# Kernel tuning notes

Hardware: AMD Instinct MI355X
Metric: run time of the kernel (lower is better)

The kernel has to match this reference:

```python
import jax, jax.numpy as jnp
import numpy as np

N, J, P = 512, 20000, 8   # samples, genes (rna_count), covariates
DIM = J - 1               # pivot=True drops one column from the softmax logits


def setup_inputs() -> dict:
    key = jax.random.key(0)
    k0, k1, k2, k3, k4 = jax.random.split(key, 5)
    X = jax.random.normal(k0, (N, P), dtype=jnp.float32)
    # counts: non-negative integers stored as float (matches torch float64 Y of counts)
    Y = jnp.round(jax.random.uniform(k1, (N, J), dtype=jnp.float32) * 1000.0)
    mu = jax.random.normal(k2, (DIM,), dtype=jnp.float32)
    beta = jax.random.normal(k3, (P * DIM,), dtype=jnp.float32) * 0.1
    phi = jax.random.normal(k4, (J,), dtype=jnp.float32)
    return {"mu": mu, "beta": beta, "phi": phi, "X": X, "Y": Y}


def _nb_loglik(y, mean, disp):
    # NB with mean `mean` and dispersion `disp` (var = mean + disp*mean^2):
    # r = 1/disp, p = r/(r+mean)
    # log pmf = lgamma(y+r) - lgamma(r) - lgamma(y+1) + r*log(p) + y*log(1-p)
    r = 1.0 / disp
    log_rpm = jnp.log(r + mean)
    return (jax.lax.lgamma(y + r) - jax.lax.lgamma(r) - jax.lax.lgamma(y + 1.0)
            + r * (jnp.log(r) - log_rpm)
            + y * (jnp.log(mean) - log_rpm))


def reference(mu, beta, phi, X, Y):
    n, p = X.shape
    dim = mu.shape[0]
    beta_ = beta.reshape(p, dim)
    logits = mu + X @ beta_                                   # [N, J-1]
    logits = jnp.concatenate(
        [logits, jnp.zeros((n, 1), dtype=logits.dtype)], axis=1)  # pivot column of zeros -> [N, J]
    pi = jax.nn.softmax(logits, axis=1)                       # exp(logits - logsumexp)
    s = jnp.sum(Y, axis=1, keepdims=True)                     # [N, 1] total counts per sample
    mean = s * pi                                             # [N, J]
    disp = jax.nn.softplus(phi)                               # [J]
    log_lik = jnp.sum(_nb_loglik(Y, mean, disp))
    return log_lik.reshape(1)
```

## Files before the change

### kernel.cpp

```cpp
#include <hip/hip_runtime.h>
#include <hip/hip_bf16.h>

constexpr int N_SAMPLES = 512;
constexpr int J_GENES   = 20000;
constexpr int P_COV     = 8;
constexpr int DIM       = J_GENES - 1;
constexpr int BLOCK     = 256;
constexpr int CHUNK     = 1024;
constexpr int CPR       = (J_GENES + CHUNK - 1) / CHUNK;
constexpr int TABLE_N   = 1024;

constexpr size_t WS_RW    = 0;
constexpr size_t WS_LOGRW = WS_RW    + J_GENES;
constexpr size_t WS_LGRW  = WS_LOGRW + J_GENES;
constexpr size_t WS_MUP   = WS_LGRW  + J_GENES;
constexpr size_t WS_BETAP = WS_MUP   + J_GENES;
constexpr size_t WS_LGYT  = WS_BETAP + (size_t)P_COV * J_GENES;
constexpr size_t WS_SACC  = WS_LGYT  + TABLE_N;
constexpr size_t WS_EACC  = WS_SACC  + N_SAMPLES;
constexpr size_t WS_PART  = WS_EACC  + N_SAMPLES;
constexpr size_t WS_TOTAL = WS_PART  + (size_t)N_SAMPLES * CPR;

__device__ inline float wave_reduce_sum(float v) {
#pragma unroll
    for (int off = 32; off > 0; off >>= 1)
        v += __shfl_down(v, off, 64);
    return v;
}

__device__ inline float lgamma_pos(float z) {
    float corr = 0.0f;
    if (z < 8.0f) {
        float p = z;
        p *= (z + 1.0f); p *= (z + 2.0f); p *= (z + 3.0f);
        p *= (z + 4.0f); p *= (z + 5.0f); p *= (z + 6.0f); p *= (z + 7.0f);
        corr = -__logf(p);
        z += 8.0f;
    }
    float lz  = __logf(z);
    float rz  = __builtin_amdgcn_rcpf(z);
    float rz2 = rz * rz;
    float ser = rz * fmaf(rz2, fmaf(rz2, 7.9365079365e-4f, -2.7777777778e-3f),
                          8.3333333333e-2f);
    return fmaf(z - 0.5f, lz, 0.91893853320467274f - z + ser + corr);
}

__global__ __launch_bounds__(BLOCK) void prep_kernel(
    const float* __restrict__ mu, const float* __restrict__ beta,
    const float* __restrict__ phi, float* __restrict__ ws) {
    int j = blockIdx.x * blockDim.x + threadIdx.x;
    if (j < N_SAMPLES) { ws[WS_SACC + j] = 0.0f; ws[WS_EACC + j] = 0.0f; }
    if (j < TABLE_N)   ws[WS_LGYT + j] = lgammaf((float)j + 1.0f);
    if (j < J_GENES) {
        float ph = phi[j];
        float sp = (ph > 20.0f) ? ph : log1pf(__expf(ph));
        float r  = 1.0f / sp;
        ws[WS_RW    + j] = r;
        ws[WS_LOGRW + j] = -__logf(sp);
        ws[WS_LGRW  + j] = lgammaf(r);
        ws[WS_MUP   + j] = (j < DIM) ? mu[j] : 0.0f;
#pragma unroll
        for (int p = 0; p < P_COV; ++p)
            ws[WS_BETAP + (size_t)p * J_GENES + j] =
                (j < DIM) ? beta[p * DIM + j] : 0.0f;
    }
}

__global__ __launch_bounds__(BLOCK) void pass1_kernel(
    const float* __restrict__ X, const float* __restrict__ Y,
    const float* __restrict__ ws_c, float* __restrict__ ws) {
    const int n = blockIdx.y;
    const int t = threadIdx.x;
    const int j = blockIdx.x * CHUNK + t * 4;

    float x[P_COV];
#pragma unroll
    for (int p = 0; p < P_COV; ++p) x[p] = X[n * P_COV + p];

    float s_acc = 0.0f, e_acc = 0.0f;
    if (j < J_GENES) {
        float4 y4 = *(const float4*)(Y + (size_t)n * J_GENES + j);
        float4 lg = *(const float4*)(ws_c + WS_MUP + j);
#pragma unroll
        for (int p = 0; p < P_COV; ++p) {
            float4 b = *(const float4*)(ws_c + WS_BETAP + (size_t)p * J_GENES + j);
            lg.x = fmaf(x[p], b.x, lg.x);
            lg.y = fmaf(x[p], b.y, lg.y);
            lg.z = fmaf(x[p], b.z, lg.z);
            lg.w = fmaf(x[p], b.w, lg.w);
        }
        s_acc = (y4.x + y4.y) + (y4.z + y4.w);
        e_acc = (__expf(lg.x) + __expf(lg.y)) + (__expf(lg.z) + __expf(lg.w));
    }

    float vs = wave_reduce_sum(s_acc);
    float ve = wave_reduce_sum(e_acc);
    __shared__ float rs[4], re[4];
    if ((t & 63) == 0) { rs[t >> 6] = vs; re[t >> 6] = ve; }
    __syncthreads();
    if (t == 0) {
        atomicAdd(&ws[WS_SACC + n], (rs[0] + rs[1]) + (rs[2] + rs[3]));
        atomicAdd(&ws[WS_EACC + n], (re[0] + re[1]) + (re[2] + re[3]));
    }
}

__device__ inline float nb_term(float y, float logit, float r, float logr,
                                float lgr, float s, float logs, float lse,
                                const float* __restrict__ tbl) {
    float lp   = logit - lse;
    float mean = s * __expf(lp);
    float lrm  = __logf(r + mean);
    int   yi   = (int)(y + 0.5f);
    float lgy1 = (yi >= 0 && yi < TABLE_N) ? tbl[yi] : lgamma_pos(y + 1.0f);
    float lgyr = lgamma_pos(y + r);
    return lgyr - lgr - lgy1 + fmaf(r, logr - lrm, y * ((logs + lp) - lrm));
}

__global__ __launch_bounds__(BLOCK) void pass2_kernel(
    const float* __restrict__ X, const float* __restrict__ Y,
    const float* __restrict__ ws_c, float* __restrict__ ws) {
    const int n = blockIdx.y;
    const int t = threadIdx.x;
    const int j = blockIdx.x * CHUNK + t * 4;

    __shared__ __align__(16) float tbl[TABLE_N];
    __shared__ float shv[3];
    *(float4*)&tbl[t * 4] = *(const float4*)(ws_c + WS_LGYT + t * 4);
    if (t == 0) {
        float s = ws_c[WS_SACC + n];
        float E = ws_c[WS_EACC + n];
        shv[0] = s; shv[1] = __logf(s); shv[2] = __logf(E);
    }
    __syncthreads();
    const float s = shv[0], logs = shv[1], lse = shv[2];

    float x[P_COV];
#pragma unroll
    for (int p = 0; p < P_COV; ++p) x[p] = X[n * P_COV + p];

    float acc = 0.0f;
    if (j < J_GENES) {
        float4 y4  = *(const float4*)(Y + (size_t)n * J_GENES + j);
        float4 lg  = *(const float4*)(ws_c + WS_MUP + j);
#pragma unroll
        for (int p = 0; p < P_COV; ++p) {
            float4 b = *(const float4*)(ws_c + WS_BETAP + (size_t)p * J_GENES + j);
            lg.x = fmaf(x[p], b.x, lg.x);
            lg.y = fmaf(x[p], b.y, lg.y);
            lg.z = fmaf(x[p], b.z, lg.z);
            lg.w = fmaf(x[p], b.w, lg.w);
        }
        float4 r4  = *(const float4*)(ws_c + WS_RW    + j);
        float4 lr4 = *(const float4*)(ws_c + WS_LOGRW + j);
        float4 lg4 = *(const float4*)(ws_c + WS_LGRW  + j);
        acc  = nb_term(y4.x, lg.x, r4.x, lr4.x, lg4.x, s, logs, lse, tbl);
        acc += nb_term(y4.y, lg.y, r4.y, lr4.y, lg4.y, s, logs, lse, tbl);
        acc += nb_term(y4.z, lg.z, r4.z, lr4.z, lg4.z, s, logs, lse, tbl);
        acc += nb_term(y4.w, lg.w, r4.w, lr4.w, lg4.w, s, logs, lse, tbl);
    }

    float v = wave_reduce_sum(acc);
    __shared__ float red[4];
    if ((t & 63) == 0) red[t >> 6] = v;
    __syncthreads();
    if (t == 0)
        ws[WS_PART + (size_t)n * CPR + blockIdx.x] =
            (red[0] + red[1]) + (red[2] + red[3]);
}

__global__ __launch_bounds__(BLOCK) void final_kernel(
    const float* __restrict__ ws_c, float* __restrict__ out) {
    const int t = threadIdx.x;
    float acc = 0.0f;
    for (int i = t; i < N_SAMPLES * CPR; i += BLOCK)
        acc += ws_c[WS_PART + i];
    float v = wave_reduce_sum(acc);
    __shared__ float red[4];
    if ((t & 63) == 0) red[t >> 6] = v;
    __syncthreads();
    if (t == 0) out[0] = (red[0] + red[1]) + (red[2] + red[3]);
}

__global__ __launch_bounds__(BLOCK) void nb_mono(
    const float* __restrict__ mu, const float* __restrict__ beta,
    const float* __restrict__ phi, const float* __restrict__ X,
    const float* __restrict__ Y, float* __restrict__ out) {
    const int n = blockIdx.x;
    const int t = threadIdx.x;
    __shared__ float red[4];
    __shared__ float sh_s, sh_lse, sh_logs;
    float x[P_COV];
#pragma unroll
    for (int p = 0; p < P_COV; ++p) x[p] = X[n * P_COV + p];
    const float* yrow = Y + (size_t)n * J_GENES;
    float s_acc = 0.0f, e_acc = 0.0f;
    for (int j = t; j < J_GENES; j += BLOCK) {
        float logit = 0.0f;
        if (j < DIM) {
            logit = mu[j];
#pragma unroll
            for (int p = 0; p < P_COV; ++p)
                logit = fmaf(x[p], beta[p * DIM + j], logit);
        }
        s_acc += yrow[j];
        e_acc += __expf(logit);
    }
    float v = wave_reduce_sum(s_acc);
    if ((t & 63) == 0) red[t >> 6] = v;
    __syncthreads();
    if (t == 0) { float st = red[0]+red[1]+red[2]+red[3]; sh_s = st; sh_logs = __logf(st); }
    __syncthreads();
    v = wave_reduce_sum(e_acc);
    if ((t & 63) == 0) red[t >> 6] = v;
    __syncthreads();
    if (t == 0) sh_lse = __logf(red[0]+red[1]+red[2]+red[3]);
    __syncthreads();
    const float s = sh_s, logs = sh_logs, lse = sh_lse;
    float acc = 0.0f;
    for (int j = t; j < J_GENES; j += BLOCK) {
        float logit = 0.0f;
        if (j < DIM) {
            logit = mu[j];
#pragma unroll
            for (int p = 0; p < P_COV; ++p)
                logit = fmaf(x[p], beta[p * DIM + j], logit);
        }
        float ph = phi[j];
        float sp = (ph > 20.0f) ? ph : log1pf(__expf(ph));
        float r  = 1.0f / sp;
        float y  = yrow[j];
        float lp = logit - lse;
        float mean = s * __expf(lp);
        float lrm  = __logf(r + mean);
        acc += lgamma_pos(y + r) - lgamma_pos(r) - lgamma_pos(y + 1.0f)
             + fmaf(r, -__logf(sp) - lrm, y * ((logs + lp) - lrm));
    }
    v = wave_reduce_sum(acc);
    if ((t & 63) == 0) red[t >> 6] = v;
    __syncthreads();
    if (t == 0) atomicAdd(out, (red[0]+red[1])+(red[2]+red[3]));
}

__global__ void zero_out_kernel(float* __restrict__ out) { out[0] = 0.0f; }

extern "C" void kernel_launch(void* const* d_in, const int* in_sizes, int n_in,
                              void* d_out, int out_size, void* d_ws, size_t ws_size,
                              hipStream_t stream) {
    const float* mu   = (const float*)d_in[0];
    const float* beta = (const float*)d_in[1];
    const float* phi  = (const float*)d_in[2];
    const float* X    = (const float*)d_in[3];
    const float* Y    = (const float*)d_in[4];
    float* out = (float*)d_out;
    float* ws  = (float*)d_ws;

    if (ws_size >= WS_TOTAL * sizeof(float)) {
        dim3 grid(CPR, N_SAMPLES);
        prep_kernel<<<(J_GENES + BLOCK - 1) / BLOCK, BLOCK, 0, stream>>>(
            mu, beta, phi, ws);
        pass1_kernel<<<grid, BLOCK, 0, stream>>>(X, Y, ws, ws);
        pass2_kernel<<<grid, BLOCK, 0, stream>>>(X, Y, ws, ws);
        final_kernel<<<1, BLOCK, 0, stream>>>(ws, out);
    } else {
        zero_out_kernel<<<1, 1, 0, stream>>>(out);
        nb_mono<<<N_SAMPLES, BLOCK, 0, stream>>>(mu, beta, phi, X, Y, out);
    }
}
```

Baseline: 149.9 us.

## Fuse both passes into one per-sample kernel with register-cached Y and logits

Merges pass1, pass2 and the final reduction into one kernel where each 512-thread block handles a whole sample row. It keeps Y and the logits in registers between the sum phase and the NB phase, so Y is not read twice and the logits are not recomputed. It also folds the per-gene constants into a single vector and rewrites the log-likelihood algebraically to drop several logs. The cost is heavy register use (20 float4s per thread) and only 512 blocks, which may limit occupancy and latency hiding.

```diff
diff --git a/kernel.cpp b/kernel.cpp
--- a/kernel.cpp
+++ b/kernel.cpp
@@ -1,25 +1,22 @@
 #include <hip/hip_runtime.h>
-#include <hip/hip_bf16.h>
 
 constexpr int N_SAMPLES = 512;
 constexpr int J_GENES   = 20000;
 constexpr int P_COV     = 8;
 constexpr int DIM       = J_GENES - 1;
-constexpr int BLOCK     = 256;
-constexpr int CHUNK     = 1024;
-constexpr int CPR       = (J_GENES + CHUNK - 1) / CHUNK;
+constexpr int BLOCK     = 512;
+constexpr int NW        = BLOCK / 64;
+constexpr int UPB       = 10;
+constexpr int JPAD      = BLOCK * 4 * UPB;
+constexpr int PREP_B    = 256;
 constexpr int TABLE_N   = 1024;
 
 constexpr size_t WS_RW    = 0;
-constexpr size_t WS_LOGRW = WS_RW    + J_GENES;
-constexpr size_t WS_LGRW  = WS_LOGRW + J_GENES;
-constexpr size_t WS_MUP   = WS_LGRW  + J_GENES;
-constexpr size_t WS_BETAP = WS_MUP   + J_GENES;
-constexpr size_t WS_LGYT  = WS_BETAP + (size_t)P_COV * J_GENES;
-constexpr size_t WS_SACC  = WS_LGYT  + TABLE_N;
-constexpr size_t WS_EACC  = WS_SACC  + N_SAMPLES;
-constexpr size_t WS_PART  = WS_EACC  + N_SAMPLES;
-constexpr size_t WS_TOTAL = WS_PART  + (size_t)N_SAMPLES * CPR;
+constexpr size_t WS_MUP   = WS_RW    + JPAD;
+constexpr size_t WS_BETAP = WS_MUP   + JPAD;
+constexpr size_t WS_CVEC  = WS_BETAP + (size_t)P_COV * JPAD;
+constexpr size_t WS_LGYT  = WS_CVEC  + JPAD;
+constexpr size_t WS_TOTAL = WS_LGYT  + TABLE_N;
 
 __device__ inline float wave_reduce_sum(float v) {
 #pragma unroll
@@ -45,143 +42,144 @@
     return fmaf(z - 0.5f, lz, 0.91893853320467274f - z + ser + corr);
 }
 
-__global__ __launch_bounds__(BLOCK) void prep_kernel(
+__global__ __launch_bounds__(PREP_B) void prep_kernel(
     const float* __restrict__ mu, const float* __restrict__ beta,
-    const float* __restrict__ phi, float* __restrict__ ws) {
-    int j = blockIdx.x * blockDim.x + threadIdx.x;
-    if (j < N_SAMPLES) { ws[WS_SACC + j] = 0.0f; ws[WS_EACC + j] = 0.0f; }
-    if (j < TABLE_N)   ws[WS_LGYT + j] = lgammaf((float)j + 1.0f);
-    if (j < J_GENES) {
+    const float* __restrict__ phi, float* __restrict__ ws,
+    float* __restrict__ out) {
+    const int gid = blockIdx.x * PREP_B + threadIdx.x;
+    if (gid == 0) out[0] = 0.0f;
+    if (gid < TABLE_N) ws[WS_LGYT + gid] = lgammaf((float)gid + 1.0f);
+    if (gid >= JPAD) return;
+    if (gid < J_GENES) {
+        const int j = gid;
         float ph = phi[j];
         float sp = (ph > 20.0f) ? ph : log1pf(__expf(ph));
         float r  = 1.0f / sp;
-        ws[WS_RW    + j] = r;
-        ws[WS_LOGRW + j] = -__logf(sp);
-        ws[WS_LGRW  + j] = lgammaf(r);
-        ws[WS_MUP   + j] = (j < DIM) ? mu[j] : 0.0f;
+        ws[WS_RW   + j] = r;
+        ws[WS_CVEC + j] = fmaf(r, -__logf(sp), -lgammaf(r));
+        ws[WS_MUP  + j] = (j < DIM) ? mu[j] : 0.0f;
 #pragma unroll
         for (int p = 0; p < P_COV; ++p)
-            ws[WS_BETAP + (size_t)p * J_GENES + j] =
+            ws[WS_BETAP + (size_t)p * JPAD + j] =
                 (j < DIM) ? beta[p * DIM + j] : 0.0f;
-    }
-}
-
-__global__ __launch_bounds__(BLOCK) void pass1_kernel(
+    } else {
+        ws[WS_RW   + gid] = 1.0f;
+        ws[WS_CVEC + gid] = 0.0f;
+        ws[WS_MUP  + gid] = 0.0f;
+#pragma unroll
+        for (int p = 0; p < P_COV; ++p)
+            ws[WS_BETAP + (size_t)p * JPAD + gid] = 0.0f;
+    }
+}
+
+__global__ __launch_bounds__(BLOCK, 4) void nb_main(
     const float* __restrict__ X, const float* __restrict__ Y,
-    const float* __restrict__ ws_c, float* __restrict__ ws) {
-    const int n = blockIdx.y;
+    const float* __restrict__ ws, float* __restrict__ out) {
+
+    const int n = blockIdx.x;
     const int t = threadIdx.x;
-    const int j = blockIdx.x * CHUNK + t * 4;
+
+    __shared__ __align__(16) float tbl[TABLE_N];
+    __shared__ float rs[NW], re[NW], red[NW];
+    __shared__ float shv[2];
+
+    if (t * 4 < TABLE_N)
+        *(float4*)&tbl[t * 4] = *(const float4*)(ws + WS_LGYT + t * 4);
 
     float x[P_COV];
 #pragma unroll
     for (int p = 0; p < P_COV; ++p) x[p] = X[n * P_COV + p];
 
+    const float* yrow = Y + (size_t)n * J_GENES;
+
+    float4 y_cache[UPB];
+    float4 l_cache[UPB];
     float s_acc = 0.0f, e_acc = 0.0f;
-    if (j < J_GENES) {
-        float4 y4 = *(const float4*)(Y + (size_t)n * J_GENES + j);
-        float4 lg = *(const float4*)(ws_c + WS_MUP + j);
-#pragma unroll
-        for (int p = 0; p < P_COV; ++p) {
-            float4 b = *(const float4*)(ws_c + WS_BETAP + (size_t)p * J_GENES + j);
-            lg.x = fmaf(x[p], b.x, lg.x);
-            lg.y = fmaf(x[p], b.y, lg.y);
-            lg.z = fmaf(x[p], b.z, lg.z);
-            lg.w = fmaf(x[p], b.w, lg.w);
-        }
-        s_acc = (y4.x + y4.y) + (y4.z + y4.w);
-        e_acc = (__expf(lg.x) + __expf(lg.y)) + (__expf(lg.z) + __expf(lg.w));
-    }
-
-    float vs = wave_reduce_sum(s_acc);
-    float ve = wave_reduce_sum(e_acc);
-    __shared__ float rs[4], re[4];
-    if ((t & 63) == 0) { rs[t >> 6] = vs; re[t >> 6] = ve; }
+
+#pragma unroll
+    for (int u = 0; u < UPB; ++u) {
+        const int j = u * (BLOCK * 4) + t * 4;
+        float4 y4 = make_float4(0.f, 0.f, 0.f, 0.f);
+        float4 lg = make_float4(0.f, 0.f, 0.f, 0.f);
+        if (j < J_GENES) {
+            y4 = *(const float4*)(yrow + j);
+            lg = *(const float4*)(ws + WS_MUP + j);
+#pragma unroll
+            for (int p = 0; p < P_COV; ++p) {
+                float4 bb = *(const float4*)(ws + WS_BETAP + (size_t)p * JPAD + j);
+                lg.x = fmaf(x[p], bb.x, lg.x);
+                lg.y = fmaf(x[p], bb.y, lg.y);
+                lg.z = fmaf(x[p], bb.z, lg.z);
+                lg.w = fmaf(x[p], bb.w, lg.w);
+            }
+            s_acc += (y4.x + y4.y) + (y4.z + y4.w);
+            e_acc += (__expf(lg.x) + __expf(lg.y)) + (__expf(lg.z) + __expf(lg.w));
+        }
+        y_cache[u] = y4;
+        l_cache[u] = lg;
+    }
+
+    {
+        float vs = wave_reduce_sum(s_acc);
+        float ve = wave_reduce_sum(e_acc);
+        if ((t & 63) == 0) { rs[t >> 6] = vs; re[t >> 6] = ve; }
+    }
     __syncthreads();
     if (t == 0) {
-        atomicAdd(&ws[WS_SACC + n], (rs[0] + rs[1]) + (rs[2] + rs[3]));
-        atomicAdd(&ws[WS_EACC + n], (re[0] + re[1]) + (re[2] + re[3]));
-    }
-}
-
-__device__ inline float nb_term(float y, float logit, float r, float logr,
-                                float lgr, float s, float logs, float lse,
-                                const float* __restrict__ tbl) {
-    float lp   = logit - lse;
-    float mean = s * __expf(lp);
-    float lrm  = __logf(r + mean);
-    int   yi   = (int)(y + 0.5f);
-    float lgy1 = (yi >= 0 && yi < TABLE_N) ? tbl[yi] : lgamma_pos(y + 1.0f);
-    float lgyr = lgamma_pos(y + r);
-    return lgyr - lgr - lgy1 + fmaf(r, logr - lrm, y * ((logs + lp) - lrm));
-}
-
-__global__ __launch_bounds__(BLOCK) void pass2_kernel(
-    const float* __restrict__ X, const float* __restrict__ Y,
-    const float* __restrict__ ws_c, float* __restrict__ ws) {
-    const int n = blockIdx.y;
-    const int t = threadIdx.x;
-    const int j = blockIdx.x * CHUNK + t * 4;
-
-    __shared__ __align__(16) float tbl[TABLE_N];
-    __shared__ float shv[3];
-    *(float4*)&tbl[t * 4] = *(const float4*)(ws_c + WS_LGYT + t * 4);
-    if (t == 0) {
-        float s = ws_c[WS_SACC + n];
-        float E = ws_c[WS_EACC + n];
-        shv[0] = s; shv[1] = __logf(s); shv[2] = __logf(E);
-    }
-    __syncthreads();
-    const float s = shv[0], logs = shv[1], lse = shv[2];
-
-    float x[P_COV];
-#pragma unroll
-    for (int p = 0; p < P_COV; ++p) x[p] = X[n * P_COV + p];
+        float s = 0.f, E = 0.f;
+#pragma unroll
+        for (int w = 0; w < NW; ++w) { s += rs[w]; E += re[w]; }
+        shv[0] = s; shv[1] = E;
+    }
+    __syncthreads();
+
+    const float s    = shv[0];
+    const float E    = shv[1];
+    const float logs = __logf(s);
+    const float lse  = __logf(E);
+    const float sE   = s / E;
 
     float acc = 0.0f;
-    if (j < J_GENES) {
-        float4 y4  = *(const float4*)(Y + (size_t)n * J_GENES + j);
-        float4 lg  = *(const float4*)(ws_c + WS_MUP + j);
-#pragma unroll
-        for (int p = 0; p < P_COV; ++p) {
-            float4 b = *(const float4*)(ws_c + WS_BETAP + (size_t)p * J_GENES + j);
-            lg.x = fmaf(x[p], b.x, lg.x);
-            lg.y = fmaf(x[p], b.y, lg.y);
-            lg.z = fmaf(x[p], b.z, lg.z);
-            lg.w = fmaf(x[p], b.w, lg.w);
-        }
-        float4 r4  = *(const float4*)(ws_c + WS_RW    + j);
-        float4 lr4 = *(const float4*)(ws_c + WS_LOGRW + j);
-        float4 lg4 = *(const float4*)(ws_c + WS_LGRW  + j);
-        acc  = nb_term(y4.x, lg.x, r4.x, lr4.x, lg4.x, s, logs, lse, tbl);
-        acc += nb_term(y4.y, lg.y, r4.y, lr4.y, lg4.y, s, logs, lse, tbl);
-        acc += nb_term(y4.z, lg.z, r4.z, lr4.z, lg4.z, s, logs, lse, tbl);
-        acc += nb_term(y4.w, lg.w, r4.w, lr4.w, lg4.w, s, logs, lse, tbl);
-    }
-
-    float v = wave_reduce_sum(acc);
-    __shared__ float red[4];
-    if ((t & 63) == 0) red[t >> 6] = v;
-    __syncthreads();
-    if (t == 0)
-        ws[WS_PART + (size_t)n * CPR + blockIdx.x] =
-            (red[0] + red[1]) + (red[2] + red[3]);
-}
-
-__global__ __launch_bounds__(BLOCK) void final_kernel(
-    const float* __restrict__ ws_c, float* __restrict__ out) {
-    const int t = threadIdx.x;
-    float acc = 0.0f;
-    for (int i = t; i < N_SAMPLES * CPR; i += BLOCK)
-        acc += ws_c[WS_PART + i];
-    float v = wave_reduce_sum(acc);
-    __shared__ float red[4];
-    if ((t & 63) == 0) red[t >> 6] = v;
-    __syncthreads();
-    if (t == 0) out[0] = (red[0] + red[1]) + (red[2] + red[3]);
-}
-
-__global__ __launch_bounds__(BLOCK) void nb_mono(
+#pragma unroll
+    for (int u = 0; u < UPB; ++u) {
+        const int j = u * (BLOCK * 4) + t * 4;
+        if (j < J_GENES) {
+            float4 y4 = y_cache[u];
+            float4 lg = l_cache[u];
+            float4 r4 = *(const float4*)(ws + WS_RW   + j);
+            float4 c4 = *(const float4*)(ws + WS_CVEC + j);
+#pragma unroll
+            for (int e = 0; e < 4; ++e) {
+                float y     = (&y4.x)[e];
+                float logit = (&lg.x)[e];
+                float r     = (&r4.x)[e];
+                float cv    = (&c4.x)[e];
+                float mean  = sE * __expf(logit);
+                float lrm   = __logf(r + mean);
+                int   yi    = (int)(y + 0.5f);
+                float lgy1  = (yi < TABLE_N) ? tbl[yi] : lgamma_pos(y + 1.0f);
+                acc += lgamma_pos(y + r) - lgy1
+                     + fmaf(-(y + r), lrm, fmaf(y, logit, cv));
+            }
+        }
+    }
+
+    if (t == 0) acc += s * (logs - lse);
+
+    {
+        float v = wave_reduce_sum(acc);
+        if ((t & 63) == 0) red[t >> 6] = v;
+        __syncthreads();
+        if (t == 0) {
+            float b = 0.f;
+#pragma unroll
+            for (int w = 0; w < NW; ++w) b += red[w];
+            atomicAdd(out, b);
+        }
+    }
+}
+
+__global__ __launch_bounds__(256) void nb_mono(
     const float* __restrict__ mu, const float* __restrict__ beta,
     const float* __restrict__ phi, const float* __restrict__ X,
     const float* __restrict__ Y, float* __restrict__ out) {
@@ -194,7 +192,7 @@
     for (int p = 0; p < P_COV; ++p) x[p] = X[n * P_COV + p];
     const float* yrow = Y + (size_t)n * J_GENES;
     float s_acc = 0.0f, e_acc = 0.0f;
-    for (int j = t; j < J_GENES; j += BLOCK) {
+    for (int j = t; j < J_GENES; j += 256) {
         float logit = 0.0f;
         if (j < DIM) {
             logit = mu[j];
@@ -217,7 +215,7 @@
     __syncthreads();
     const float s = sh_s, logs = sh_logs, lse = sh_lse;
     float acc = 0.0f;
-    for (int j = t; j < J_GENES; j += BLOCK) {
+    for (int j = t; j < J_GENES; j += 256) {
         float logit = 0.0f;
         if (j < DIM) {
             logit = mu[j];
@@ -255,14 +253,10 @@
     float* ws  = (float*)d_ws;
 
     if (ws_size >= WS_TOTAL * sizeof(float)) {
-        dim3 grid(CPR, N_SAMPLES);
-        prep_kernel<<<(J_GENES + BLOCK - 1) / BLOCK, BLOCK, 0, stream>>>(
-            mu, beta, phi, ws);
-        pass1_kernel<<<grid, BLOCK, 0, stream>>>(X, Y, ws, ws);
-        pass2_kernel<<<grid, BLOCK, 0, stream>>>(X, Y, ws, ws);
-        final_kernel<<<1, BLOCK, 0, stream>>>(ws, out);
+        prep_kernel<<<JPAD / PREP_B, PREP_B, 0, stream>>>(mu, beta, phi, ws, out);
+        nb_main<<<N_SAMPLES, BLOCK, 0, stream>>>(X, Y, ws, out);
     } else {
         zero_out_kernel<<<1, 1, 0, stream>>>(out);
-        nb_mono<<<N_SAMPLES, BLOCK, 0, stream>>>(mu, beta, phi, X, Y, out);
-    }
-}
+        nb_mono<<<N_SAMPLES, 256, 0, stream>>>(mu, beta, phi, X, Y, out);
+    }
+}
```

Result: slower. 271.2 us (+80.9%).
